# Optimization experiments

Measured on AMD Instinct MI355X. Metric: run time of the kernel, lower is better.

## Reference

```python
import jax, jax.numpy as jnp
import numpy as np

B, L, F = 8, 4096, 80
D, H, NB = 512, 2048, 4
EPS = 1e-5


def _p(k, shape, fan_in):
    return jax.random.normal(k, shape, dtype=jnp.float32) / np.float32(np.sqrt(fan_in))


def setup_inputs() -> dict:
    ks = iter(jax.random.split(jax.random.key(0), 32))
    c1, c2, c3 = D // 4, D // 2, D
    f1 = (F - 1) // 2 + 1
    f_out = (f1 - 1) // 2 + 1  # freq dim after two stride-2 convs = 20
    inp = {}
    inp["x"] = jax.random.normal(next(ks), (B, L, F), dtype=jnp.float32)
    inp["x_len"] = jax.random.randint(next(ks), (B,), L // 2, L + 1, dtype=jnp.int32)
    inp["conv1_w"] = _p(next(ks), (c1, 1, 3, 3), 9.0)
    inp["conv1_b"] = jnp.zeros((c1,), jnp.float32)
    inp["conv2_w"] = _p(next(ks), (c2, c1, 3, 3), 9.0 * c1)
    inp["conv2_b"] = jnp.zeros((c2,), jnp.float32)
    inp["conv3_w"] = _p(next(ks), (c3, c2, 3, 3), 9.0 * c2)
    inp["conv3_b"] = jnp.zeros((c3,), jnp.float32)
    inp["embed_w"] = _p(next(ks), (c3 * f_out, D), c3 * f_out)
    inp["embed_b"] = jnp.zeros((D,), jnp.float32)
    inp["embed_ln_g"] = jnp.ones((D,), jnp.float32)
    inp["embed_ln_b"] = jnp.zeros((D,), jnp.float32)
    inp["ln_att_g"] = jnp.ones((NB, D), jnp.float32)
    inp["ln_att_b"] = jnp.zeros((NB, D), jnp.float32)
    inp["att_decay"] = jax.random.normal(next(ks), (NB, D), dtype=jnp.float32) * 0.5 - 1.0
    inp["att_first"] = jax.random.normal(next(ks), (NB, D), dtype=jnp.float32) * 0.5
    inp["att_mix_k"] = jax.random.uniform(next(ks), (NB, D), dtype=jnp.float32)
    inp["att_mix_v"] = jax.random.uniform(next(ks), (NB, D), dtype=jnp.float32)
    inp["att_mix_r"] = jax.random.uniform(next(ks), (NB, D), dtype=jnp.float32)
    inp["att_wk"] = _p(next(ks), (NB, D, D), D)
    inp["att_wv"] = _p(next(ks), (NB, D, D), D)
    inp["att_wr"] = _p(next(ks), (NB, D, D), D)
    inp["att_wo"] = _p(next(ks), (NB, D, D), D)
    inp["ln_ffn_g"] = jnp.ones((NB, D), jnp.float32)
    inp["ln_ffn_b"] = jnp.zeros((NB, D), jnp.float32)
    inp["ffn_mix_k"] = jax.random.uniform(next(ks), (NB, D), dtype=jnp.float32)
    inp["ffn_mix_r"] = jax.random.uniform(next(ks), (NB, D), dtype=jnp.float32)
    inp["ffn_wk"] = _p(next(ks), (NB, D, H), D)
    inp["ffn_wv"] = _p(next(ks), (NB, H, D), H)
    inp["ffn_wr"] = _p(next(ks), (NB, D, D), D)
    inp["final_ln_g"] = jnp.ones((D,), jnp.float32)
    inp["final_ln_b"] = jnp.zeros((D,), jnp.float32)
    return inp


def _ln(x, g, b):
    m = jnp.mean(x, axis=-1, keepdims=True)
    v = jnp.var(x, axis=-1, keepdims=True)
    return (x - m) * jax.lax.rsqrt(v + EPS) * g + b


def _shift(x):  # (B,U,D): x_{t-1}, zeros at t=0 (torch ZeroPad2d((0,0,1,-1)))
    return jnp.pad(x, ((0, 0), (1, 0), (0, 0)))[:, :-1, :]


def _conv(x, w, b, stride):
    y = jax.lax.conv_general_dilated(x, w, stride, [(1, 1), (1, 1)],
                                     dimension_numbers=("NCHW", "OIHW", "NCHW"))
    return jax.nn.relu(y + b[None, :, None, None])


def _wkv(w, u, k, v):
    # Numerically-stable RWKV-4 WKV linear attention. w,u: (D,); k,v: (B,U,D).
    Bb, U, Dd = k.shape
    def step(carry, kv):
        aa, bb, pp = carry
        kt, vt = kv
        ww = u + kt
        p = jnp.maximum(pp, ww)
        e1 = jnp.exp(pp - p)
        e2 = jnp.exp(ww - p)
        out = (e1 * aa + e2 * vt) / (e1 * bb + e2)
        ww2 = pp + w
        p2 = jnp.maximum(ww2, kt)
        e1 = jnp.exp(ww2 - p2)
        e2 = jnp.exp(kt - p2)
        return (e1 * aa + e2 * vt, e1 * bb + e2, p2), out
    init = (jnp.zeros((Bb, Dd), k.dtype), jnp.zeros((Bb, Dd), k.dtype),
            jnp.full((Bb, Dd), -1e38, k.dtype))
    _, out = jax.lax.scan(step, init, (jnp.moveaxis(k, 1, 0), jnp.moveaxis(v, 1, 0)))
    return jnp.moveaxis(out, 0, 1)


def reference(x, x_len, conv1_w, conv1_b, conv2_w, conv2_b, conv3_w, conv3_b,
              embed_w, embed_b, embed_ln_g, embed_ln_b,
              ln_att_g, ln_att_b, att_decay, att_first,
              att_mix_k, att_mix_v, att_mix_r, att_wk, att_wv, att_wr, att_wo,
              ln_ffn_g, ln_ffn_b, ffn_mix_k, ffn_mix_r, ffn_wk, ffn_wv, ffn_wr,
              final_ln_g, final_ln_b):
    # conv frontend: (B,L,F) -> (B,U=L//4,D)
    y = _conv(x[:, None], conv1_w, conv1_b, (2, 2))
    y = _conv(y, conv2_w, conv2_b, (2, 2))
    y = _conv(y, conv3_w, conv3_b, (1, 1))
    Bb, C, U, Fo = y.shape
    y = jnp.transpose(y, (0, 2, 1, 3)).reshape(Bb, U, C * Fo)
    h = _ln(y @ embed_w + embed_b, embed_ln_g, embed_ln_b)
    for i in range(NB):
        # time mixing (WKV attention)
        xn = _ln(h, ln_att_g[i], ln_att_b[i])
        sh = _shift(xn)
        k = (xn * att_mix_k[i] + sh * (1.0 - att_mix_k[i])) @ att_wk[i]
        v = (xn * att_mix_v[i] + sh * (1.0 - att_mix_v[i])) @ att_wv[i]
        r = jax.nn.sigmoid((xn * att_mix_r[i] + sh * (1.0 - att_mix_r[i])) @ att_wr[i])
        wkv = _wkv(-jnp.exp(att_decay[i]), att_first[i], k, v)
        h = h + (r * wkv) @ att_wo[i]
        # channel mixing (FFN)
        xn = _ln(h, ln_ffn_g[i], ln_ffn_b[i])
        sh = _shift(xn)
        kk = jnp.square(jax.nn.relu((xn * ffn_mix_k[i] + sh * (1.0 - ffn_mix_k[i])) @ ffn_wk[i]))
        rr = jax.nn.sigmoid((xn * ffn_mix_r[i] + sh * (1.0 - ffn_mix_r[i])) @ ffn_wr[i])
        h = h + rr * (kk @ ffn_wv[i])
    h = _ln(h, final_ln_g, final_ln_b)
    l1 = (x_len - 1) // 2 + 1
    olens = (l1 - 1) // 2 + 1
    return h, olens
```

## Files before the change

kernel.cpp:

```cpp
#include <hip/hip_runtime.h>
#include <hip/hip_bf16.h>
#include <hip/hip_fp8.h>

typedef __hip_bfloat16 bf16;
typedef __bf16 v8bf __attribute__((ext_vector_type(8)));
typedef float v4f __attribute__((ext_vector_type(4)));
typedef unsigned short u16x8 __attribute__((ext_vector_type(8)));


constexpr int B_T = 0, B_CONV = 1;
constexpr int EP_CONV_CL = 0, EP_CONV_T = 1, EP_ATOMIC = 2, EP_KVR = 3,
              EP_ADD = 4, EP_FFN = 5, EP_ADDMUL = 6;

constexpr int WC = 64;
constexpr int WT = 1024 / WC;
constexpr int WPLANE = WC * 4096;

static __device__ __forceinline__ unsigned short f2b(float f) {
    return __builtin_bit_cast(unsigned short, __float2bfloat16(f));
}
static __device__ __forceinline__ unsigned char f2e4(float f) {
    __hip_fp8_e4m3 q(f);
    return (unsigned char)q.__x;
}

static __device__ __forceinline__ void gld16(const unsigned char* g,
                                             unsigned char* l) {
    __builtin_amdgcn_global_load_lds(
        (__attribute__((address_space(1))) void*)g,
        (__attribute__((address_space(3))) void*)l, 16, 0, 0);
}

template <int TM, int BL, int EPM, int ASH, int TIN, int FIN, int STRIDE,
          int ICN, int HALO, int F8>
__global__ __launch_bounds__(256) void gemm_k(
    const void* __restrict__ Av, const void* __restrict__ Bwv,
    const void* __restrict__ Bactv,
    float* __restrict__ C, void* __restrict__ Cbv,
    const float* __restrict__ bias, const float* __restrict__ mul,
    int M, int N, int K, int KLEN, float wsc)
{
    constexpr int MI = TM / 32;
    constexpr int ESZ = F8 ? 1 : 2;
    constexpr int BKe = 64 / ESZ;
    __shared__ __align__(16) unsigned char As[3][TM * 64];
    __shared__ __align__(16) unsigned char Bs[3][128 * 64];
    const unsigned char* A    = (const unsigned char*)Av;
    const unsigned char* Bw   = (const unsigned char*)Bwv;
    const unsigned char* Bact = (const unsigned char*)Bactv;
    const int tid = threadIdx.x;
    const int n0 = blockIdx.x * 128;
    const int m0 = blockIdx.y * TM;
    const int kbase = blockIdx.z * KLEN;
    const int wave = tid >> 6, lane = tid & 63;
    const int wr = wave >> 1, wc = wave & 1;
    const int lq = lane >> 4, lr = lane & 15;

    if constexpr (ASH > 0) A += (size_t)(n0 >> ASH) * M * K * ESZ;

    v4f acc[MI][4];
#pragma unroll
    for (int i = 0; i < MI; i++)
#pragma unroll
        for (int j = 0; j < 4; j++) acc[i][j] = v4f{0.f, 0.f, 0.f, 0.f};

    const int sr = tid >> 2;
    const int swzB = ((tid & 3) ^ ((tid >> 3) & 3)) * 16;

    const unsigned char* aP[TM / 64];
#pragma unroll
    for (int c = 0; c < TM / 64; c++)
        aP[c] = A + (size_t)(m0 + c * 64 + sr) * K * ESZ + swzB;

    const unsigned char* bP[2];
    int cb0 = 0, cb1 = 0, cto0 = 0, cto1 = 0, cfo0 = 0, cfo1 = 0;
    if constexpr (BL == B_T) {
#pragma unroll
        for (int c = 0; c < 2; c++)
            bP[c] = Bw + (size_t)(n0 + c * 64 + sr) * K * ESZ + swzB;
    } else {
        {
            int n = n0 + sr;
            cb0 = n / 20480;
            int s = n - cb0 * 20480;
            cto0 = s / 20;
            cfo0 = s - cto0 * 20;
        }
        {
            int n = n0 + 64 + sr;
            cb1 = n / 20480;
            int s = n - cb1 * 20480;
            cto1 = s / 20;
            cfo1 = s - cto1 * 20;
        }
        if constexpr (HALO) {
            bP[0] = Bact + ((((size_t)cb0 * 1026 + cto0) * 22 + cfo0) * 256) * ESZ + swzB;
            bP[1] = Bact + ((((size_t)cb1 * 1026 + cto1) * 22 + cfo1) * 256) * ESZ + swzB;
        }
    }

    auto stageA = [&](int k0, int sel) {
#pragma unroll
        for (int c = 0; c < TM / 64; c++)
            gld16(aP[c] + (size_t)k0 * ESZ, &As[sel][c * 4096 + wave * 1024]);
    };
    auto stageB = [&](int k0, int sel) {
        if constexpr (BL == B_T) {
#pragma unroll
            for (int c = 0; c < 2; c++)
                gld16(bP[c] + (size_t)k0 * ESZ, &Bs[sel][c * 4096 + wave * 1024]);
        } else {
            int kg = k0 / ICN;
            int ic0 = k0 - kg * ICN;
            int kt = kg / 3, kf = kg - kt * 3;
            if constexpr (HALO) {
                gld16(bP[0] + ((size_t)(kt * 22 + kf) * 256 + ic0) * ESZ,
                      &Bs[sel][wave * 1024]);
                gld16(bP[1] + ((size_t)(kt * 22 + kf) * 256 + ic0) * ESZ,
                      &Bs[sel][4096 + wave * 1024]);
            } else {
                int ti0 = cto0 * STRIDE - 1 + kt, fi0 = cfo0 * STRIDE - 1 + kf;
                const unsigned char* s0 =
                    ((unsigned)ti0 < (unsigned)TIN && (unsigned)fi0 < (unsigned)FIN)
                    ? Bact + ((((size_t)cb0 * TIN + ti0) * FIN + fi0) * ICN + ic0) * ESZ + swzB
                    : Bw;
                gld16(s0, &Bs[sel][wave * 1024]);
                int ti1 = cto1 * STRIDE - 1 + kt, fi1 = cfo1 * STRIDE - 1 + kf;
                const unsigned char* s1 =
                    ((unsigned)ti1 < (unsigned)TIN && (unsigned)fi1 < (unsigned)FIN)
                    ? Bact + ((((size_t)cb1 * TIN + ti1) * FIN + fi1) * ICN + ic0) * ESZ + swzB
                    : Bw;
                gld16(s1, &Bs[sel][4096 + wave * 1024]);
            }
        }
    };
    auto compute = [&](int sel) {
        if constexpr (F8) {
            const int so2 = ((lr >> 1) & 3) << 1;
            long fa8[MI][2], fb8[4][2];
#pragma unroll
            for (int mi = 0; mi < MI; mi++)
#pragma unroll
                for (int kk = 0; kk < 2; kk++)
                    fa8[mi][kk] = *(const long*)&As[sel][
                        (wr * (TM / 2) + mi * 16 + lr) * 64 +
                        (((kk << 2) | lq) ^ so2) * 8];
#pragma unroll
            for (int ni = 0; ni < 4; ni++)
#pragma unroll
                for (int kk = 0; kk < 2; kk++)
                    fb8[ni][kk] = *(const long*)&Bs[sel][
                        (wc * 64 + ni * 16 + lr) * 64 +
                        (((kk << 2) | lq) ^ so2) * 8];
#pragma unroll
            for (int mi = 0; mi < MI; mi++)
#pragma unroll
                for (int ni = 0; ni < 4; ni++) {
                    acc[mi][ni] = __builtin_amdgcn_mfma_f32_16x16x32_fp8_fp8(
                        fa8[mi][0], fb8[ni][0], acc[mi][ni], 0, 0, 0);
                    acc[mi][ni] = __builtin_amdgcn_mfma_f32_16x16x32_fp8_fp8(
                        fa8[mi][1], fb8[ni][1], acc[mi][ni], 0, 0, 0);
                }
        } else {
            const int lsw = (lr >> 1) & 3;
            v8bf fa[MI], fb[4];
#pragma unroll
            for (int mi = 0; mi < MI; mi++)
                fa[mi] = *(const v8bf*)&As[sel][(wr * (TM / 2) + mi * 16 + lr) * 64 +
                                               (lq ^ lsw) * 16];
#pragma unroll
            for (int ni = 0; ni < 4; ni++)
                fb[ni] = *(const v8bf*)&Bs[sel][(wc * 64 + ni * 16 + lr) * 64 +
                                               (lq ^ lsw) * 16];
#pragma unroll
            for (int mi = 0; mi < MI; mi++)
#pragma unroll
                for (int ni = 0; ni < 4; ni++)
                    acc[mi][ni] = __builtin_amdgcn_mfma_f32_16x16x32_bf16(
                        fa[mi], fb[ni], acc[mi][ni], 0, 0, 0);
        }
    };

    const int NT = KLEN / BKe;
    stageA(kbase, 0);            stageB(kbase, 0);
    stageA(kbase + BKe, 1);      stageB(kbase + BKe, 1);
    stageA(kbase + 2 * BKe, 2);  stageB(kbase + 2 * BKe, 2);
    int sel = 0;
    for (int t = 0; t < NT - 2; ++t) {
        if constexpr (TM == 128)
            asm volatile("s_waitcnt vmcnt(8)" ::: "memory");
        else
            asm volatile("s_waitcnt vmcnt(6)" ::: "memory");
        __builtin_amdgcn_sched_barrier(0);
        __builtin_amdgcn_s_barrier();
        compute(sel);
        __builtin_amdgcn_s_barrier();
        if (t + 3 < NT) {
            int k0 = kbase + (t + 3) * BKe;
            stageA(k0, sel);
            stageB(k0, sel);
        }
        sel = sel == 2 ? 0 : sel + 1;
    }
    if constexpr (TM == 128)
        asm volatile("s_waitcnt vmcnt(4)" ::: "memory");
    else
        asm volatile("s_waitcnt vmcnt(3)" ::: "memory");
    __builtin_amdgcn_sched_barrier(0);
    __builtin_amdgcn_s_barrier();
    compute(sel);
    sel = sel == 2 ? 0 : sel + 1;
    asm volatile("s_waitcnt vmcnt(0)" ::: "memory");
    __builtin_amdgcn_sched_barrier(0);
    __builtin_amdgcn_s_barrier();
    compute(sel);

#pragma unroll
    for (int mi = 0; mi < MI; mi++) {
#pragma unroll
        for (int ni = 0; ni < 4; ni++) {
#pragma unroll
            for (int reg = 0; reg < 4; reg++) {
                int row = m0 + wr * (TM / 2) + mi * 16 + lq * 4 + reg;
                int col = n0 + wc * 64 + ni * 16 + lr;
                float v = acc[mi][ni][reg] * wsc;
                if constexpr (EPM == EP_CONV_CL) {
                    v += bias[row];
                    v = v > 0.f ? v : 0.f;
                    int b = col / 20480;
                    int s = col - b * 20480;
                    int t = s / 20, fo = s - t * 20;
                    ((unsigned char*)Cbv)[(((size_t)b * 1026 + t + 1) * 22 + fo + 1) * 256 + row] =
                        f2e4(v);
                } else if constexpr (EPM == EP_CONV_T) {
                    v += bias[row];
                    v = v > 0.f ? v : 0.f;
                    int b = col / 20480;
                    int s = col - b * 20480;
                    int t = s / 20, fo = s - t * 20;
                    ((unsigned char*)Cbv)[(size_t)(b * 1024 + t) * 10240 + row * 20 + fo] =
                        f2e4(v);
                } else if constexpr (EPM == EP_ATOMIC) {
                    float add = (blockIdx.z == 0) ? bias[col] : 0.f;
                    atomicAdd(&C[(size_t)row * N + col], v + add);
                } else if constexpr (EPM == EP_KVR) {
                    int seg = col >> 9;
                    if (seg == 2) v = 1.f / (1.f + __expf(-v));
                    C[(size_t)seg * M * 512 + (size_t)row * 512 + (col & 511)] = v;
                } else if constexpr (EPM == EP_ADD) {
                    C[(size_t)row * N + col] += v;
                } else if constexpr (EPM == EP_FFN) {
                    if (col < 2048) {
                        float t = v > 0.f ? v : 0.f;
                        ((bf16*)Cbv)[(size_t)row * 2048 + col] = __float2bfloat16(t * t);
                    } else {
                        C[(size_t)row * 512 + (col - 2048)] = 1.f / (1.f + __expf(-v));
                    }
                } else if constexpr (EPM == EP_ADDMUL) {
                    size_t idx = (size_t)row * N + col;
                    C[idx] += mul[idx] * v;
                }
            }
        }
    }
}

__global__ __launch_bounds__(256) void reorder_w8_k(const float* __restrict__ in,
                                                    unsigned char* __restrict__ out,
                                                    int OC, int IC)
{
    int idx = blockIdx.x * 256 + threadIdx.x;
    if (idx >= OC * IC * 9) return;
    int oc = idx / (IC * 9);
    int r = idx - oc * (IC * 9);
    int g = r / IC;
    int ic = r - g * IC;
    out[idx] = f2e4(in[((size_t)oc * IC + ic) * 9 + g] * 16.f);
}

__global__ __launch_bounds__(256) void transpose_k(const float* __restrict__ in,
                                                   bf16* __restrict__ out,
                                                   int K, int N, size_t ozs)
{
    __shared__ float t[32][33];
    const float* pin = in + (size_t)blockIdx.z * K * N;
    bf16* pout = out + (size_t)blockIdx.z * ozs;
    int n0 = blockIdx.x * 32, k0 = blockIdx.y * 32;
    int tx = threadIdx.x & 31, ty = threadIdx.x >> 5;
#pragma unroll
    for (int i = 0; i < 32; i += 8)
        t[ty + i][tx] = pin[(size_t)(k0 + ty + i) * N + n0 + tx];
    __syncthreads();
#pragma unroll
    for (int i = 0; i < 32; i += 8)
        pout[(size_t)(n0 + ty + i) * K + k0 + tx] = __float2bfloat16(t[tx][ty + i]);
}

__global__ __launch_bounds__(256) void transpose8_k(const float* __restrict__ in,
                                                    unsigned char* __restrict__ out,
                                                    int K, int N)
{
    __shared__ float t[32][33];
    int n0 = blockIdx.x * 32, k0 = blockIdx.y * 32;
    int tx = threadIdx.x & 31, ty = threadIdx.x >> 5;
#pragma unroll
    for (int i = 0; i < 32; i += 8)
        t[ty + i][tx] = in[(size_t)(k0 + ty + i) * N + n0 + tx];
    __syncthreads();
#pragma unroll
    for (int i = 0; i < 32; i += 8)
        out[(size_t)(n0 + ty + i) * K + k0 + tx] = f2e4(t[tx][ty + i] * 64.f);
}

__global__ __launch_bounds__(256) void conv1_k(
    const float* __restrict__ x, const float* __restrict__ w,
    const float* __restrict__ bias, unsigned char* __restrict__ out)
{
    __shared__ float ws_[128 * 9];
    __shared__ float bs_[128];
    const int tid = threadIdx.x;
    for (int i = tid; i < 128 * 9; i += 256) ws_[i] = w[i];
    if (tid < 128) bs_[tid] = bias[tid];
    __syncthreads();

    int idx = blockIdx.x * 256 + tid;
    int f = idx % 40;
    int t = (idx / 40) & 2047;
    int b = idx / 81920;

    float xin[9];
#pragma unroll
    for (int kt = 0; kt < 3; kt++)
#pragma unroll
        for (int kf = 0; kf < 3; kf++) {
            int ti = 2 * t - 1 + kt, fi = 2 * f - 1 + kf;
            float v = 0.f;
            if ((unsigned)ti < 4096u && (unsigned)fi < 80u)
                v = x[(size_t)b * 327680 + (size_t)ti * 80 + fi];
            xin[kt * 3 + kf] = v;
        }
    unsigned char* outu = out + (size_t)idx * 128;
#pragma unroll
    for (int oc8 = 0; oc8 < 16; oc8++) {
        unsigned char pk[8];
#pragma unroll
        for (int j = 0; j < 8; j++) {
            int oc = oc8 * 8 + j;
            float a = bs_[oc];
#pragma unroll
            for (int q = 0; q < 9; q++) a += ws_[oc * 9 + q] * xin[q];
            a = a > 0.f ? a : 0.f;
            pk[j] = f2e4(a);
        }
        *(unsigned long long*)&outu[oc8 * 8] = *(unsigned long long*)pk;
    }
}

__global__ __launch_bounds__(256) void ln_k(
    const float* __restrict__ in, float* __restrict__ out,
    const float* __restrict__ g, const float* __restrict__ b, int M)
{
    int wave = threadIdx.x >> 6;
    int lane = threadIdx.x & 63;
    int row = blockIdx.x * 4 + wave;
    if (row >= M) return;
    const float* p = in + (size_t)row * 512;
    float v[8], s = 0.f, sq = 0.f;
#pragma unroll
    for (int i = 0; i < 8; i++) {
        v[i] = p[lane + i * 64];
        s += v[i];
        sq += v[i] * v[i];
    }
#pragma unroll
    for (int o = 32; o > 0; o >>= 1) {
        s += __shfl_xor(s, o, 64);
        sq += __shfl_xor(sq, o, 64);
    }
    float mean = s * (1.f / 512.f);
    float var = sq * (1.f / 512.f) - mean * mean;
    float r = rsqrtf(var + 1e-5f);
    float* q = out + (size_t)row * 512;
#pragma unroll
    for (int i = 0; i < 8; i++) {
        int d = lane + i * 64;
        q[d] = (v[i] - mean) * r * g[d] + b[d];
    }
}

template <int NOUT>
__global__ __launch_bounds__(256) void lnmix_k(
    const float* __restrict__ hb, const float* __restrict__ g,
    const float* __restrict__ b, const float* __restrict__ mk,
    const float* __restrict__ mv, const float* __restrict__ mr,
    bf16* __restrict__ ok, bf16* __restrict__ ov, bf16* __restrict__ orr)
{
    int wave = threadIdx.x >> 6, lane = threadIdx.x & 63;
    int row = blockIdx.x * 4 + wave;
    int u = row & 1023;
    int d0 = lane * 8;
    const float* pc = hb + (size_t)row * 512 + d0;

    float vc[8], vp[8];
    *(float4*)&vc[0] = *(const float4*)pc;
    *(float4*)&vc[4] = *(const float4*)(pc + 4);
    float s = 0.f, sq = 0.f, sp = 0.f, sqp = 0.f;
#pragma unroll
    for (int i = 0; i < 8; i++) { s += vc[i]; sq += vc[i] * vc[i]; }
    if (u) {
        *(float4*)&vp[0] = *(const float4*)(pc - 512);
        *(float4*)&vp[4] = *(const float4*)(pc - 508);
#pragma unroll
        for (int i = 0; i < 8; i++) { sp += vp[i]; sqp += vp[i] * vp[i]; }
    } else {
#pragma unroll
        for (int i = 0; i < 8; i++) vp[i] = 0.f;
    }
#pragma unroll
    for (int o = 32; o > 0; o >>= 1) {
        s += __shfl_xor(s, o, 64);
        sq += __shfl_xor(sq, o, 64);
        sp += __shfl_xor(sp, o, 64);
        sqp += __shfl_xor(sqp, o, 64);
    }
    float mc = s * (1.f / 512.f);
    float rc = rsqrtf(sq * (1.f / 512.f) - mc * mc + 1e-5f);
    float mp = sp * (1.f / 512.f);
    float rp = rsqrtf(sqp * (1.f / 512.f) - mp * mp + 1e-5f);

    float gv[8], bv[8], xc[8], xp[8];
    *(float4*)&gv[0] = *(const float4*)(g + d0);
    *(float4*)&gv[4] = *(const float4*)(g + d0 + 4);
    *(float4*)&bv[0] = *(const float4*)(b + d0);
    *(float4*)&bv[4] = *(const float4*)(b + d0 + 4);
#pragma unroll
    for (int i = 0; i < 8; i++) {
        xc[i] = (vc[i] - mc) * rc * gv[i] + bv[i];
        xp[i] = u ? (vp[i] - mp) * rp * gv[i] + bv[i] : 0.f;
    }

    size_t ob = (size_t)row * 512 + d0;
    float a[8];
    unsigned short o16[8];
    *(float4*)&a[0] = *(const float4*)(mk + d0);
    *(float4*)&a[4] = *(const float4*)(mk + d0 + 4);
#pragma unroll
    for (int i = 0; i < 8; i++) o16[i] = f2b(xc[i] * a[i] + xp[i] * (1.f - a[i]));
    *(u16x8*)((unsigned short*)ok + ob) = *(u16x8*)o16;
    if constexpr (NOUT == 3) {
        *(float4*)&a[0] = *(const float4*)(mv + d0);
        *(float4*)&a[4] = *(const float4*)(mv + d0 + 4);
#pragma unroll
        for (int i = 0; i < 8; i++) o16[i] = f2b(xc[i] * a[i] + xp[i] * (1.f - a[i]));
        *(u16x8*)((unsigned short*)ov + ob) = *(u16x8*)o16;
    }
    *(float4*)&a[0] = *(const float4*)(mr + d0);
    *(float4*)&a[4] = *(const float4*)(mr + d0 + 4);
#pragma unroll
    for (int i = 0; i < 8; i++) o16[i] = f2b(xc[i] * a[i] + xp[i] * (1.f - a[i]));
    *(u16x8*)((unsigned short*)orr + ob) = *(u16x8*)o16;
}

__global__ __launch_bounds__(256) void wkv_loc_k(
    const float* __restrict__ kbuf, const float* __restrict__ vbuf,
    float* __restrict__ st, const float* __restrict__ decay)
{
    int idx = blockIdx.x * 256 + threadIdx.x;
    int bd = idx & 4095;
    int c = idx >> 12;
    int d = bd & 511;
    int b = bd >> 9;
    float w = -__expf(decay[d]);
    float aa = 0.f, bb = 0.f, pp = -1e38f;
    size_t base = ((size_t)b * 1024 + c * WT) * 512 + d;
#pragma unroll
    for (int s = 0; s < WT; s++) {
        float kt = kbuf[base + (size_t)s * 512];
        float vt = vbuf[base + (size_t)s * 512];
        float ww2 = pp + w;
        float p2 = ww2 > kt ? ww2 : kt;
        float e1 = __expf(ww2 - p2), e2 = __expf(kt - p2);
        aa = e1 * aa + e2 * vt;
        bb = e1 * bb + e2;
        pp = p2;
    }
    st[idx] = aa;
    st[WPLANE + idx] = bb;
    st[2 * WPLANE + idx] = pp;
}

__global__ __launch_bounds__(256) void wkv_comb_k(
    const float* __restrict__ loc, float* __restrict__ inc,
    const float* __restrict__ decay)
{
    int bd = blockIdx.x * 256 + threadIdx.x;
    int d = bd & 511;
    float wT = -__expf(decay[d]) * (float)WT;
    float aa = 0.f, bb = 0.f, pp = -1e38f;
    for (int c = 0; c < WC; c++) {
        int i = c * 4096 + bd;
        inc[i] = aa;
        inc[WPLANE + i] = bb;
        inc[2 * WPLANE + i] = pp;
        float la = loc[i], lb = loc[WPLANE + i], lp = loc[2 * WPLANE + i];
        float pd = pp + wT;
        float p2 = pd > lp ? pd : lp;
        float e1 = __expf(pd - p2), e2 = __expf(lp - p2);
        aa = e1 * aa + e2 * la;
        bb = e1 * bb + e2 * lb;
        pp = p2;
    }
}

__global__ __launch_bounds__(256) void wkv_out_k(
    const float* __restrict__ kbuf, const float* __restrict__ vbuf,
    const float* __restrict__ rbuf, bf16* __restrict__ outbuf,
    const float* __restrict__ inc,
    const float* __restrict__ decay, const float* __restrict__ first)
{
    int idx = blockIdx.x * 256 + threadIdx.x;
    int bd = idx & 4095;
    int c = idx >> 12;
    int d = bd & 511;
    int b = bd >> 9;
    float w = -__expf(decay[d]);
    float u = first[d];
    float aa = inc[idx], bb = inc[WPLANE + idx], pp = inc[2 * WPLANE + idx];
    size_t base = ((size_t)b * 1024 + c * WT) * 512 + d;
#pragma unroll
    for (int s = 0; s < WT; s++) {
        float kt = kbuf[base + (size_t)s * 512];
        float vt = vbuf[base + (size_t)s * 512];
        float rt = rbuf[base + (size_t)s * 512];
        float ww = u + kt;
        float p = pp > ww ? pp : ww;
        float e1 = __expf(pp - p), e2 = __expf(ww - p);
        float out = (e1 * aa + e2 * vt) / (e1 * bb + e2);
        outbuf[base + (size_t)s * 512] = __float2bfloat16(rt * out);
        float ww2 = pp + w;
        float p2 = ww2 > kt ? ww2 : kt;
        e1 = __expf(ww2 - p2);
        e2 = __expf(kt - p2);
        aa = e1 * aa + e2 * vt;
        bb = e1 * bb + e2;
        pp = p2;
    }
}

__global__ void olens_k(const int* __restrict__ x_len, float* __restrict__ out)
{
    int i = threadIdx.x;
    if (i < 8) {
        int l1 = (x_len[i] - 1) / 2 + 1;
        int ol = (l1 - 1) / 2 + 1;
        out[i] = (float)ol;
    }
}

extern "C" void kernel_launch(void* const* d_in, const int* in_sizes, int n_in,
                              void* d_out, int out_size, void* d_ws, size_t ws_size,
                              hipStream_t stream)
{
    (void)in_sizes; (void)n_in; (void)out_size; (void)ws_size;
    const float* x         = (const float*)d_in[0];
    const int*   x_len     = (const int*)d_in[1];
    const float* conv1_w   = (const float*)d_in[2];
    const float* conv1_b   = (const float*)d_in[3];
    const float* conv2_w   = (const float*)d_in[4];
    const float* conv2_b   = (const float*)d_in[5];
    const float* conv3_w   = (const float*)d_in[6];
    const float* conv3_b   = (const float*)d_in[7];
    const float* embed_w   = (const float*)d_in[8];
    const float* embed_b   = (const float*)d_in[9];
    const float* embed_ln_g= (const float*)d_in[10];
    const float* embed_ln_b= (const float*)d_in[11];
    const float* ln_att_g  = (const float*)d_in[12];
    const float* ln_att_b  = (const float*)d_in[13];
    const float* att_decay = (const float*)d_in[14];
    const float* att_first = (const float*)d_in[15];
    const float* att_mix_k = (const float*)d_in[16];
    const float* att_mix_v = (const float*)d_in[17];
    const float* att_mix_r = (const float*)d_in[18];
    const float* att_wk    = (const float*)d_in[19];
    const float* att_wv    = (const float*)d_in[20];
    const float* att_wr    = (const float*)d_in[21];
    const float* att_wo    = (const float*)d_in[22];
    const float* ln_ffn_g  = (const float*)d_in[23];
    const float* ln_ffn_b  = (const float*)d_in[24];
    const float* ffn_mix_k = (const float*)d_in[25];
    const float* ffn_mix_r = (const float*)d_in[26];
    const float* ffn_wk    = (const float*)d_in[27];
    const float* ffn_wv    = (const float*)d_in[28];
    const float* ffn_wr    = (const float*)d_in[29];
    const float* final_ln_g= (const float*)d_in[30];
    const float* final_ln_b= (const float*)d_in[31];

    char* wsb = (char*)d_ws;
    float* h     = (float*)(wsb);
    float* xn    = (float*)(wsb + (16LL << 20));
    float* sloc  = (float*)(wsb + (16LL << 20));
    float* sinc  = (float*)(wsb + (20LL << 20));
    bf16*  rwkvb = (bf16*) (wsb + (32LL << 20));
    bf16*  xkvr  = (bf16*) (wsb + (40LL << 20));
    bf16*  xf    = xkvr;
    float* kvrb  = (float*)(wsb + (64LL << 20));
    bf16*  kkb   = (bf16*) (wsb + (112LL << 20));
    unsigned char* c1b  = (unsigned char*)(wsb + (40LL << 20));
    unsigned char* c2b  = (unsigned char*)(wsb + (80LL << 20));
    unsigned char* zpg  = (unsigned char*)(wsb + (103LL << 20));
    unsigned char* c3b  = (unsigned char*)(wsb + (104LL << 20));
    bf16*  attT  = (bf16*) (wsb + (144LL << 20));
    bf16*  attTo = (bf16*) (wsb + (150LL << 20));
    bf16*  ffnT  = (bf16*) (wsb + (152LL << 20));
    bf16*  ffnTv = (bf16*) (wsb + (162LL << 20));
    unsigned char* embT = (unsigned char*)(wsb + (170LL << 20));
    unsigned char* c2wb = (unsigned char*)(wsb + (180LL << 20));
    unsigned char* c3wb = (unsigned char*)(wsb + (180LL << 20) + 294912);

    const size_t MD = 8192LL * 512;

    transpose_k<<<dim3(16, 16, 4), 256, 0, stream>>>(att_wk, attT, 512, 512, 786432);
    transpose_k<<<dim3(16, 16, 4), 256, 0, stream>>>(att_wv, attT + 262144, 512, 512, 786432);
    transpose_k<<<dim3(16, 16, 4), 256, 0, stream>>>(att_wr, attT + 524288, 512, 512, 786432);
    transpose_k<<<dim3(16, 16, 4), 256, 0, stream>>>(att_wo, attTo, 512, 512, 262144);
    transpose_k<<<dim3(64, 16, 4), 256, 0, stream>>>(ffn_wk, ffnT, 512, 2048, 1310720);
    transpose_k<<<dim3(16, 16, 4), 256, 0, stream>>>(ffn_wr, ffnT + 1048576, 512, 512, 1310720);
    transpose_k<<<dim3(16, 64, 4), 256, 0, stream>>>(ffn_wv, ffnTv, 2048, 512, 1048576);
    transpose8_k<<<dim3(16, 320), 256, 0, stream>>>(embed_w, embT, 10240, 512);
    reorder_w8_k<<<1152, 256, 0, stream>>>(conv2_w, c2wb, 256, 128);
    reorder_w8_k<<<4608, 256, 0, stream>>>(conv3_w, c3wb, 512, 256);
    hipMemsetAsync(xn, 0, 16LL << 20, stream);
    hipMemsetAsync(c2b, 0, 2LL * 1026 * 22 * 256, stream);
    hipMemsetAsync(zpg, 0, 4096, stream);

    for (int chunk = 0; chunk < 4; chunk++) {
        int b0 = chunk * 2;
        conv1_k<<<640, 256, 0, stream>>>(x + (size_t)b0 * 327680, conv1_w, conv1_b, c1b);
        gemm_k<128, B_CONV, EP_CONV_CL, 0, 2048, 40, 2, 128, 0, 1><<<dim3(320, 2), 256, 0, stream>>>(
            c2wb, zpg, c1b, nullptr, c2b, conv2_b, nullptr,
            256, 40960, 1152, 1152, 0.0625f);
        gemm_k<128, B_CONV, EP_CONV_T, 0, 1024, 20, 1, 256, 1, 1><<<dim3(320, 4), 256, 0, stream>>>(
            c3wb, nullptr, c2b, nullptr, c3b, conv3_b, nullptr,
            512, 40960, 2304, 2304, 0.0625f);
        gemm_k<64, B_T, EP_ATOMIC, 0, 0, 0, 0, 0, 0, 1><<<dim3(4, 32, 4), 256, 0, stream>>>(
            c3b, embT, nullptr, xn + (size_t)b0 * 1024 * 512, nullptr, embed_b, nullptr,
            2048, 512, 10240, 2560, 0.015625f);
    }
    ln_k<<<2048, 256, 0, stream>>>(xn, h, embed_ln_g, embed_ln_b, 8192);

    for (int i = 0; i < 4; i++) {
        lnmix_k<3><<<2048, 256, 0, stream>>>(h, ln_att_g + i * 512, ln_att_b + i * 512,
                                             att_mix_k + i * 512, att_mix_v + i * 512,
                                             att_mix_r + i * 512,
                                             xkvr, xkvr + MD, xkvr + 2 * MD);
        gemm_k<64, B_T, EP_KVR, 9, 0, 0, 0, 0, 0, 0><<<dim3(12, 128), 256, 0, stream>>>(
            xkvr, attT + (size_t)i * 786432, nullptr, kvrb, nullptr, nullptr, nullptr,
            8192, 1536, 512, 512, 1.f);
        wkv_loc_k<<<1024, 256, 0, stream>>>(kvrb, kvrb + MD, sloc, att_decay + i * 512);
        wkv_comb_k<<<16, 256, 0, stream>>>(sloc, sinc, att_decay + i * 512);
        wkv_out_k<<<1024, 256, 0, stream>>>(kvrb, kvrb + MD, kvrb + 2 * MD, rwkvb,
                                            sinc, att_decay + i * 512, att_first + i * 512);
        gemm_k<64, B_T, EP_ADD, 0, 0, 0, 0, 0, 0, 0><<<dim3(4, 128), 256, 0, stream>>>(
            rwkvb, attTo + (size_t)i * 262144, nullptr, h, nullptr, nullptr, nullptr,
            8192, 512, 512, 512, 1.f);
        lnmix_k<2><<<2048, 256, 0, stream>>>(h, ln_ffn_g + i * 512, ln_ffn_b + i * 512,
                                             ffn_mix_k + i * 512, nullptr,
                                             ffn_mix_r + i * 512,
                                             xf, nullptr, xf + MD);
        gemm_k<64, B_T, EP_FFN, 11, 0, 0, 0, 0, 0, 0><<<dim3(20, 128), 256, 0, stream>>>(
            xf, ffnT + (size_t)i * 1310720, nullptr, kvrb + 2 * MD, kkb, nullptr, nullptr,
            8192, 2560, 512, 512, 1.f);
        gemm_k<64, B_T, EP_ADDMUL, 0, 0, 0, 0, 0, 0, 0><<<dim3(4, 128), 256, 0, stream>>>(
            kkb, ffnTv + (size_t)i * 1048576, nullptr, h, nullptr, nullptr, kvrb + 2 * MD,
            8192, 512, 2048, 2048, 1.f);
    }

    ln_k<<<2048, 256, 0, stream>>>(h, (float*)d_out, final_ln_g, final_ln_b, 8192);
    olens_k<<<1, 64, 0, stream>>>(x_len, (float*)d_out + 4194304);
}
```

Baseline: 1.645 ms.

## Switch all transformer-block GEMMs from bf16 to fp8 e4m3 operands

```diff
diff --git a/kernel.cpp b/kernel.cpp
--- a/kernel.cpp
+++ b/kernel.cpp
@@ -65,7 +65,10 @@
         for (int j = 0; j < 4; j++) acc[i][j] = v4f{0.f, 0.f, 0.f, 0.f};
 
     const int sr = tid >> 2;
-    const int swzB = ((tid & 3) ^ ((tid >> 3) & 3)) * 16;
+    int fT;
+    if constexpr (F8) fT = (((tid >> 3) & 3) ^ ((tid >> 5) & 1));
+    else              fT = ((tid >> 3) & 3);
+    const int swzB = ((tid & 3) ^ fT) * 16;
 
     const unsigned char* aP[TM / 64];
 #pragma unroll
@@ -136,7 +139,7 @@
     };
     auto compute = [&](int sel) {
         if constexpr (F8) {
-            const int so2 = ((lr >> 1) & 3) << 1;
+            const int so2 = ((((lr >> 1) & 3) ^ ((lr >> 3) & 1)) << 1);
             long fa8[MI][2], fb8[4][2];
 #pragma unroll
             for (int mi = 0; mi < MI; mi++)
@@ -252,7 +255,7 @@
                 } else if constexpr (EPM == EP_FFN) {
                     if (col < 2048) {
                         float t = v > 0.f ? v : 0.f;
-                        ((bf16*)Cbv)[(size_t)row * 2048 + col] = __float2bfloat16(t * t);
+                        ((unsigned char*)Cbv)[(size_t)row * 2048 + col] = f2e4(t * t);
                     } else {
                         C[(size_t)row * 512 + (col - 2048)] = 1.f / (1.f + __expf(-v));
                     }
@@ -278,13 +281,14 @@
     out[idx] = f2e4(in[((size_t)oc * IC + ic) * 9 + g] * 16.f);
 }
 
-__global__ __launch_bounds__(256) void transpose_k(const float* __restrict__ in,
-                                                   bf16* __restrict__ out,
-                                                   int K, int N, size_t ozs)
+__global__ __launch_bounds__(256) void transpose8_k(const float* __restrict__ in,
+                                                    unsigned char* __restrict__ out,
+                                                    int K, int N, size_t izs,
+                                                    size_t ozs, float sc)
 {
     __shared__ float t[32][33];
-    const float* pin = in + (size_t)blockIdx.z * K * N;
-    bf16* pout = out + (size_t)blockIdx.z * ozs;
+    const float* pin = in + (size_t)blockIdx.z * izs;
+    unsigned char* pout = out + (size_t)blockIdx.z * ozs;
     int n0 = blockIdx.x * 32, k0 = blockIdx.y * 32;
     int tx = threadIdx.x & 31, ty = threadIdx.x >> 5;
 #pragma unroll
@@ -293,23 +297,7 @@
     __syncthreads();
 #pragma unroll
     for (int i = 0; i < 32; i += 8)
-        pout[(size_t)(n0 + ty + i) * K + k0 + tx] = __float2bfloat16(t[tx][ty + i]);
-}
-
-__global__ __launch_bounds__(256) void transpose8_k(const float* __restrict__ in,
-                                                    unsigned char* __restrict__ out,
-                                                    int K, int N)
-{
-    __shared__ float t[32][33];
-    int n0 = blockIdx.x * 32, k0 = blockIdx.y * 32;
-    int tx = threadIdx.x & 31, ty = threadIdx.x >> 5;
-#pragma unroll
-    for (int i = 0; i < 32; i += 8)
-        t[ty + i][tx] = in[(size_t)(k0 + ty + i) * N + n0 + tx];
-    __syncthreads();
-#pragma unroll
-    for (int i = 0; i < 32; i += 8)
-        out[(size_t)(n0 + ty + i) * K + k0 + tx] = f2e4(t[tx][ty + i] * 64.f);
+        pout[(size_t)(n0 + ty + i) * K + k0 + tx] = f2e4(t[tx][ty + i] * sc);
 }
 
 __global__ __launch_bounds__(256) void conv1_k(
@@ -393,7 +381,8 @@
     const float* __restrict__ hb, const float* __restrict__ g,
     const float* __restrict__ b, const float* __restrict__ mk,
     const float* __restrict__ mv, const float* __restrict__ mr,
-    bf16* __restrict__ ok, bf16* __restrict__ ov, bf16* __restrict__ orr)
+    unsigned char* __restrict__ ok, unsigned char* __restrict__ ov,
+    unsigned char* __restrict__ orr)
 {
     int wave = threadIdx.x >> 6, lane = threadIdx.x & 63;
     int row = blockIdx.x * 4 + wave;
@@ -441,24 +430,24 @@
 
     size_t ob = (size_t)row * 512 + d0;
     float a[8];
-    unsigned short o16[8];
+    unsigned char o8[8];
     *(float4*)&a[0] = *(const float4*)(mk + d0);
     *(float4*)&a[4] = *(const float4*)(mk + d0 + 4);
 #pragma unroll
-    for (int i = 0; i < 8; i++) o16[i] = f2b(xc[i] * a[i] + xp[i] * (1.f - a[i]));
-    *(u16x8*)((unsigned short*)ok + ob) = *(u16x8*)o16;
+    for (int i = 0; i < 8; i++) o8[i] = f2e4(xc[i] * a[i] + xp[i] * (1.f - a[i]));
+    *(unsigned long long*)(ok + ob) = *(unsigned long long*)o8;
     if constexpr (NOUT == 3) {
         *(float4*)&a[0] = *(const float4*)(mv + d0);
         *(float4*)&a[4] = *(const float4*)(mv + d0 + 4);
 #pragma unroll
-        for (int i = 0; i < 8; i++) o16[i] = f2b(xc[i] * a[i] + xp[i] * (1.f - a[i]));
-        *(u16x8*)((unsigned short*)ov + ob) = *(u16x8*)o16;
+        for (int i = 0; i < 8; i++) o8[i] = f2e4(xc[i] * a[i] + xp[i] * (1.f - a[i]));
+        *(unsigned long long*)(ov + ob) = *(unsigned long long*)o8;
     }
     *(float4*)&a[0] = *(const float4*)(mr + d0);
     *(float4*)&a[4] = *(const float4*)(mr + d0 + 4);
 #pragma unroll
-    for (int i = 0; i < 8; i++) o16[i] = f2b(xc[i] * a[i] + xp[i] * (1.f - a[i]));
-    *(u16x8*)((unsigned short*)orr + ob) = *(u16x8*)o16;
+    for (int i = 0; i < 8; i++) o8[i] = f2e4(xc[i] * a[i] + xp[i] * (1.f - a[i]));
+    *(unsigned long long*)(orr + ob) = *(unsigned long long*)o8;
 }
 
 __global__ __launch_bounds__(256) void wkv_loc_k(
@@ -514,7 +503,7 @@
 
 __global__ __launch_bounds__(256) void wkv_out_k(
     const float* __restrict__ kbuf, const float* __restrict__ vbuf,
-    const float* __restrict__ rbuf, bf16* __restrict__ outbuf,
+    const float* __restrict__ rbuf, unsigned char* __restrict__ outbuf,
     const float* __restrict__ inc,
     const float* __restrict__ decay, const float* __restrict__ first)
 {
@@ -536,7 +525,7 @@
         float p = pp > ww ? pp : ww;
         float e1 = __expf(pp - p), e2 = __expf(ww - p);
         float out = (e1 * aa + e2 * vt) / (e1 * bb + e2);
-        outbuf[base + (size_t)s * 512] = __float2bfloat16(rt * out);
+        outbuf[base + (size_t)s * 512] = f2e4(rt * out);
         float ww2 = pp + w;
         float p2 = ww2 > kt ? ww2 : kt;
         e1 = __expf(ww2 - p2);
@@ -600,33 +589,42 @@
     float* xn    = (float*)(wsb + (16LL << 20));
     float* sloc  = (float*)(wsb + (16LL << 20));
     float* sinc  = (float*)(wsb + (20LL << 20));
-    bf16*  rwkvb = (bf16*) (wsb + (32LL << 20));
-    bf16*  xkvr  = (bf16*) (wsb + (40LL << 20));
-    bf16*  xf    = xkvr;
+    unsigned char* rwkv8 = (unsigned char*)(wsb + (32LL << 20));
+    unsigned char* xkvr8 = (unsigned char*)(wsb + (40LL << 20));
+    unsigned char* xf8   = xkvr8;
     float* kvrb  = (float*)(wsb + (64LL << 20));
-    bf16*  kkb   = (bf16*) (wsb + (112LL << 20));
+    unsigned char* kkb8  = (unsigned char*)(wsb + (112LL << 20));
     unsigned char* c1b  = (unsigned char*)(wsb + (40LL << 20));
     unsigned char* c2b  = (unsigned char*)(wsb + (80LL << 20));
     unsigned char* zpg  = (unsigned char*)(wsb + (103LL << 20));
     unsigned char* c3b  = (unsigned char*)(wsb + (104LL << 20));
-    bf16*  attT  = (bf16*) (wsb + (144LL << 20));
-    bf16*  attTo = (bf16*) (wsb + (150LL << 20));
-    bf16*  ffnT  = (bf16*) (wsb + (152LL << 20));
-    bf16*  ffnTv = (bf16*) (wsb + (162LL << 20));
-    unsigned char* embT = (unsigned char*)(wsb + (170LL << 20));
+    unsigned char* attT8  = (unsigned char*)(wsb + (144LL << 20));
+    unsigned char* attTo8 = (unsigned char*)(wsb + (150LL << 20));
+    unsigned char* ffnT8  = (unsigned char*)(wsb + (152LL << 20));
+    unsigned char* ffnTv8 = (unsigned char*)(wsb + (162LL << 20));
+    unsigned char* embT8  = (unsigned char*)(wsb + (170LL << 20));
     unsigned char* c2wb = (unsigned char*)(wsb + (180LL << 20));
     unsigned char* c3wb = (unsigned char*)(wsb + (180LL << 20) + 294912);
 
-    const size_t MD = 8192LL * 512;
-
-    transpose_k<<<dim3(16, 16, 4), 256, 0, stream>>>(att_wk, attT, 512, 512, 786432);
-    transpose_k<<<dim3(16, 16, 4), 256, 0, stream>>>(att_wv, attT + 262144, 512, 512, 786432);
-    transpose_k<<<dim3(16, 16, 4), 256, 0, stream>>>(att_wr, attT + 524288, 512, 512, 786432);
-    transpose_k<<<dim3(16, 16, 4), 256, 0, stream>>>(att_wo, attTo, 512, 512, 262144);
-    transpose_k<<<dim3(64, 16, 4), 256, 0, stream>>>(ffn_wk, ffnT, 512, 2048, 1310720);
-    transpose_k<<<dim3(16, 16, 4), 256, 0, stream>>>(ffn_wr, ffnT + 1048576, 512, 512, 1310720);
-    transpose_k<<<dim3(16, 64, 4), 256, 0, stream>>>(ffn_wv, ffnTv, 2048, 512, 1048576);
-    transpose8_k<<<dim3(16, 320), 256, 0, stream>>>(embed_w, embT, 10240, 512);
+    const size_t MD  = 8192LL * 512;
+    const size_t MD8 = 8192LL * 512;
+
+    transpose8_k<<<dim3(16, 16, 4), 256, 0, stream>>>(att_wk, attT8, 512, 512,
+                                                      262144, 786432, 16.f);
+    transpose8_k<<<dim3(16, 16, 4), 256, 0, stream>>>(att_wv, attT8 + 262144, 512, 512,
+                                                      262144, 786432, 16.f);
+    transpose8_k<<<dim3(16, 16, 4), 256, 0, stream>>>(att_wr, attT8 + 524288, 512, 512,
+                                                      262144, 786432, 16.f);
+    transpose8_k<<<dim3(16, 16, 4), 256, 0, stream>>>(att_wo, attTo8, 512, 512,
+                                                      262144, 262144, 16.f);
+    transpose8_k<<<dim3(64, 16, 4), 256, 0, stream>>>(ffn_wk, ffnT8, 512, 2048,
+                                                      1048576, 1310720, 16.f);
+    transpose8_k<<<dim3(16, 16, 4), 256, 0, stream>>>(ffn_wr, ffnT8 + 1048576, 512, 512,
+                                                      262144, 1310720, 16.f);
+    transpose8_k<<<dim3(16, 64, 4), 256, 0, stream>>>(ffn_wv, ffnTv8, 2048, 512,
+                                                      1048576, 1048576, 16.f);
+    transpose8_k<<<dim3(16, 320, 1), 256, 0, stream>>>(embed_w, embT8, 10240, 512,
+                                                       0, 0, 64.f);
     reorder_w8_k<<<1152, 256, 0, stream>>>(conv2_w, c2wb, 256, 128);
     reorder_w8_k<<<4608, 256, 0, stream>>>(conv3_w, c3wb, 512, 256);
     hipMemsetAsync(xn, 0, 16LL << 20, stream);
@@ -643,7 +641,7 @@
             c3wb, nullptr, c2b, nullptr, c3b, conv3_b, nullptr,
             512, 40960, 2304, 2304, 0.0625f);
         gemm_k<64, B_T, EP_ATOMIC, 0, 0, 0, 0, 0, 0, 1><<<dim3(4, 32, 4), 256, 0, stream>>>(
-            c3b, embT, nullptr, xn + (size_t)b0 * 1024 * 512, nullptr, embed_b, nullptr,
+            c3b, embT8, nullptr, xn + (size_t)b0 * 1024 * 512, nullptr, embed_b, nullptr,
             2048, 512, 10240, 2560, 0.015625f);
     }
     ln_k<<<2048, 256, 0, stream>>>(xn, h, embed_ln_g, embed_ln_b, 8192);
@@ -652,27 +650,27 @@
         lnmix_k<3><<<2048, 256, 0, stream>>>(h, ln_att_g + i * 512, ln_att_b + i * 512,
                                              att_mix_k + i * 512, att_mix_v + i * 512,
                                              att_mix_r + i * 512,
-                                             xkvr, xkvr + MD, xkvr + 2 * MD);
-        gemm_k<64, B_T, EP_KVR, 9, 0, 0, 0, 0, 0, 0><<<dim3(12, 128), 256, 0, stream>>>(
-            xkvr, attT + (size_t)i * 786432, nullptr, kvrb, nullptr, nullptr, nullptr,
-            8192, 1536, 512, 512, 1.f);
+                                             xkvr8, xkvr8 + MD8, xkvr8 + 2 * MD8);
+        gemm_k<64, B_T, EP_KVR, 9, 0, 0, 0, 0, 0, 1><<<dim3(12, 128), 256, 0, stream>>>(
+            xkvr8, attT8 + (size_t)i * 786432, nullptr, kvrb, nullptr, nullptr, nullptr,
+            8192, 1536, 512, 512, 0.0625f);
         wkv_loc_k<<<1024, 256, 0, stream>>>(kvrb, kvrb + MD, sloc, att_decay + i * 512);
         wkv_comb_k<<<16, 256, 0, stream>>>(sloc, sinc, att_decay + i * 512);
-        wkv_out_k<<<1024, 256, 0, stream>>>(kvrb, kvrb + MD, kvrb + 2 * MD, rwkvb,
+        wkv_out_k<<<1024, 256, 0, stream>>>(kvrb, kvrb + MD, kvrb + 2 * MD, rwkv8,
                                             sinc, att_decay + i * 512, att_first + i * 512);
-        gemm_k<64, B_T, EP_ADD, 0, 0, 0, 0, 0, 0, 0><<<dim3(4, 128), 256, 0, stream>>>(
-            rwkvb, attTo + (size_t)i * 262144, nullptr, h, nullptr, nullptr, nullptr,
-            8192, 512, 512, 512, 1.f);
+        gemm_k<64, B_T, EP_ADD, 0, 0, 0, 0, 0, 0, 1><<<dim3(4, 128), 256, 0, stream>>>(
+            rwkv8, attTo8 + (size_t)i * 262144, nullptr, h, nullptr, nullptr, nullptr,
+            8192, 512, 512, 512, 0.0625f);
         lnmix_k<2><<<2048, 256, 0, stream>>>(h, ln_ffn_g + i * 512, ln_ffn_b + i * 512,
                                              ffn_mix_k + i * 512, nullptr,
                                              ffn_mix_r + i * 512,
-                                             xf, nullptr, xf + MD);
-        gemm_k<64, B_T, EP_FFN, 11, 0, 0, 0, 0, 0, 0><<<dim3(20, 128), 256, 0, stream>>>(
-            xf, ffnT + (size_t)i * 1310720, nullptr, kvrb + 2 * MD, kkb, nullptr, nullptr,
-            8192, 2560, 512, 512, 1.f);
-        gemm_k<64, B_T, EP_ADDMUL, 0, 0, 0, 0, 0, 0, 0><<<dim3(4, 128), 256, 0, stream>>>(
-            kkb, ffnTv + (size_t)i * 1048576, nullptr, h, nullptr, nullptr, kvrb + 2 * MD,
-            8192, 512, 2048, 2048, 1.f);
+                                             xf8, nullptr, xf8 + MD8);
+        gemm_k<64, B_T, EP_FFN, 11, 0, 0, 0, 0, 0, 1><<<dim3(20, 128), 256, 0, stream>>>(
+            xf8, ffnT8 + (size_t)i * 1310720, nullptr, kvrb + 2 * MD, kkb8, nullptr, nullptr,
+            8192, 2560, 512, 512, 0.0625f);
+        gemm_k<64, B_T, EP_ADDMUL, 0, 0, 0, 0, 0, 0, 1><<<dim3(4, 128), 256, 0, stream>>>(
+            kkb8, ffnTv8 + (size_t)i * 1048576, nullptr, h, nullptr, nullptr, kvrb + 2 * MD,
+            8192, 512, 2048, 2048, 0.0625f);
     }
 
     ln_k<<<2048, 256, 0, stream>>>(h, (float*)d_out, final_ln_g, final_ln_b, 8192);
```

Measured after the change: 1.519 ms. 7.7% less time.
